# Kernel tuning notes

Hardware: AMD Instinct MI355X
Metric: run time of the kernel (lower is better)

The kernel has to match this reference:

```python
import jax, jax.numpy as jnp
import numpy as np

# DLMLayer (breadth=2) forward, soft/dense path.
# Group arities: 0 (nullary [B,C0]), 1 (unary [B,n,C1]), 2 (binary [B,n,n,C2]).
# Per group i: concat [Expand(inputs[i-1]), inputs[i], Reduce(inputs[i+1])],
# then Permutation(i) (concat over i! axis permutations), then logic MLP
# (Linear -> sigmoid) over the channel dim. exclude_self masks the diagonal
# in the binary->unary reduction (max filled with 0, min filled with 1,
# valid for probabilistic truth values in [0,1]).

def setup_inputs() -> dict:
    key = jax.random.key(0)
    ks = jax.random.split(key, 9)
    B, n, C = 16, 128, 64
    x0 = jax.random.uniform(ks[0], (B, 8), dtype=jnp.float32)
    x1 = jax.random.uniform(ks[1], (B, n, C), dtype=jnp.float32)
    x2 = jax.random.uniform(ks[2], (B, n, n, C), dtype=jnp.float32)
    # current_dim per group: i=0: 8 + 2*64 = 136 ; i=1: 8 + 64 + 2*64 = 200 (1!=1)
    # i=2: (64 + 64) * 2! = 256
    W0 = jax.random.normal(ks[3], (136, C), dtype=jnp.float32) * 0.1
    W1 = jax.random.normal(ks[4], (200, C), dtype=jnp.float32) * 0.1
    W2 = jax.random.normal(ks[5], (256, C), dtype=jnp.float32) * 0.1
    b0 = jnp.zeros((C,), jnp.float32)
    b1 = jnp.zeros((C,), jnp.float32)
    b2 = jnp.zeros((C,), jnp.float32)
    return {"x0": x0, "x1": x1, "x2": x2, "W0": W0, "b0": b0,
            "W1": W1, "b1": b1, "W2": W2, "b2": b2}


def reference(x0, x1, x2, W0, b0, W1, b1, W2, b2):
    B, n, C = x1.shape
    # ---- group 0 (nullary): input x0 + reduce(x1) over the object axis ----
    r1 = jnp.concatenate([x1.max(axis=1), x1.min(axis=1)], axis=-1)  # [B, 2C]
    f0 = jnp.concatenate([x0, r1], axis=-1)                          # [B, 136]
    out0 = jax.nn.sigmoid(f0 @ W0 + b0)                              # [B, C]
    # ---- group 1 (unary): expand x0, input x1, reduce x2 (exclude self) ----
    e0 = jnp.broadcast_to(x0[:, None, :], (B, n, x0.shape[-1]))      # [B, n, 8]
    diag = jnp.eye(n, dtype=bool)[None, :, :, None]                  # [1, n, n, 1]
    rmax = jnp.where(diag, 0.0, x2).max(axis=2)                      # [B, n, C]
    rmin = jnp.where(diag, 1.0, x2).min(axis=2)                      # [B, n, C]
    f1 = jnp.concatenate([e0, x1, rmax, rmin], axis=-1)              # [B, n, 200]
    out1 = jax.nn.sigmoid(f1 @ W1 + b1)                              # [B, n, C]
    # ---- group 2 (binary): expand x1, input x2, permute axes (1,2) ----
    e1 = jnp.broadcast_to(x1[:, :, None, :], (B, n, n, C))           # [B, n, n, C]
    g = jnp.concatenate([e1, x2], axis=-1)                           # [B, n, n, 2C]
    f2 = jnp.concatenate([g, jnp.swapaxes(g, 1, 2)], axis=-1)        # [B, n, n, 4C]
    out2 = jax.nn.sigmoid(f2 @ W2 + b2)                              # [B, n, n, C]
    return (out0, out1, out2)
```

## Files before the change

kernel.cpp:

```cpp
#include <hip/hip_runtime.h>
#include <hip/hip_bf16.h>
#include <cstdint>


#define NDIM 128
#define CDIM 64

typedef float f32x4 __attribute__((ext_vector_type(4)));
typedef short s16x8 __attribute__((ext_vector_type(8)));

__device__ __forceinline__ unsigned short f2bf(float f) {
    union { float f; unsigned int u; } v; v.f = f;
    unsigned int u = v.u;
    return (unsigned short)((u + 0x7FFFu + ((u >> 16) & 1u)) >> 16);
}
__device__ __forceinline__ float sigmoidf_(float x) {
    return 1.0f / (1.0f + __expf(-x));
}

__global__ void prep_pab(const float* __restrict__ x1, const float* __restrict__ W2,
                         const float* __restrict__ b2,
                         float* __restrict__ PA, float* __restrict__ PB) {
    int blk = blockIdx.x;
    int c = threadIdx.x;
    __shared__ float xv[64];
    xv[c] = x1[blk * 64 + c];
    __syncthreads();
    float accA = b2[c];
    float accB = 0.f;
#pragma unroll 8
    for (int k = 0; k < 64; ++k) {
        float xk = xv[k];
        accA += xk * W2[k * 64 + c];
        accB += xk * W2[(128 + k) * 64 + c];
    }
    PA[blk * 64 + c] = accA;
    PB[blk * 64 + c] = accB;
}

__global__ void prep_wt(const float* __restrict__ W2, unsigned short* __restrict__ WT) {
    int idx = blockIdx.x * 256 + threadIdx.x;
    int n = idx >> 7, k = idx & 127;
    int row = (k < 64) ? (64 + k) : (128 + k);
    WT[idx] = f2bf(W2[row * 64 + n]);
}

__global__ __launch_bounds__(256) void k_out0(const float* __restrict__ x0,
        const float* __restrict__ x1, const float* __restrict__ W0,
        const float* __restrict__ b0, float* __restrict__ out0) {
    int b = blockIdx.x;
    int t = threadIdx.x;
    int lane = t & 63, w = t >> 6;
    int q = lane & 15;
    int jq = lane >> 4;
    __shared__ float pw[4][64], pn[4][64], f0[136], spart[4][64];

    f32x4 mx = {-1e30f, -1e30f, -1e30f, -1e30f};
    f32x4 mn = {1e30f, 1e30f, 1e30f, 1e30f};
#pragma unroll
    for (int p = 0; p < 8; ++p) {
        int j = (w * 4 + jq) + 16 * p;
        float4 v = *reinterpret_cast<const float4*>(x1 + ((size_t)(b * 128 + j)) * 64 + q * 4);
        mx.x = fmaxf(mx.x, v.x); mx.y = fmaxf(mx.y, v.y);
        mx.z = fmaxf(mx.z, v.z); mx.w = fmaxf(mx.w, v.w);
        mn.x = fminf(mn.x, v.x); mn.y = fminf(mn.y, v.y);
        mn.z = fminf(mn.z, v.z); mn.w = fminf(mn.w, v.w);
    }
#pragma unroll
    for (int d = 16; d <= 32; d <<= 1) {
        mx.x = fmaxf(mx.x, __shfl_xor(mx.x, d)); mx.y = fmaxf(mx.y, __shfl_xor(mx.y, d));
        mx.z = fmaxf(mx.z, __shfl_xor(mx.z, d)); mx.w = fmaxf(mx.w, __shfl_xor(mx.w, d));
        mn.x = fminf(mn.x, __shfl_xor(mn.x, d)); mn.y = fminf(mn.y, __shfl_xor(mn.y, d));
        mn.z = fminf(mn.z, __shfl_xor(mn.z, d)); mn.w = fminf(mn.w, __shfl_xor(mn.w, d));
    }
    if (lane < 16) {
        *reinterpret_cast<f32x4*>(&pw[w][lane * 4]) = mx;
        *reinterpret_cast<f32x4*>(&pn[w][lane * 4]) = mn;
    }
    __syncthreads();
    if (t < 64) {
        int c = t;
        float M = fmaxf(fmaxf(pw[0][c], pw[1][c]), fmaxf(pw[2][c], pw[3][c]));
        float m = fminf(fminf(pn[0][c], pn[1][c]), fminf(pn[2][c], pn[3][c]));
        f0[8 + c] = M; f0[72 + c] = m;
        if (c < 8) f0[c] = x0[b * 8 + c];
    }
    __syncthreads();
    {
        int g = t >> 6, c = t & 63;
        float acc = 0.f;
#pragma unroll
        for (int k = g * 34; k < g * 34 + 34; ++k) acc += f0[k] * W0[k * 64 + c];
        spart[g][c] = acc;
    }
    __syncthreads();
    if (t < 64) {
        int c = t;
        out0[b * 64 + c] = sigmoidf_(spart[0][c] + spart[1][c] + spart[2][c] + spart[3][c] + b0[c]);
    }
}

__global__ __launch_bounds__(256) void k_fused(const float* __restrict__ x0,
        const float* __restrict__ x1, const float* __restrict__ x2,
        const unsigned short* __restrict__ WT,
        const float* __restrict__ W1, const float* __restrict__ b1,
        const float* __restrict__ PA, const float* __restrict__ PB,
        float* __restrict__ out1, float* __restrict__ out2) {
    int blk = blockIdx.x;
    int b = blk >> 7, i = blk & 127;
    int t = threadIdx.x;
    int lane = t & 63, w = t >> 6;
    int jq = lane >> 4;
    int cc = (lane & 15) * 4;

    __shared__ __align__(16) unsigned short Ald[128 * 128];
    __shared__ float pwmax[4][64], pwmin[4][64], spart[4][64], sf[200];

    const float* xaSrc = x2 + (size_t)blk * (NDIM * CDIM);

    float4 va[8];
#pragma unroll
    for (int p = 0; p < 8; ++p) {
        int j = 32 * w + p * 4 + jq;
        va[p] = *reinterpret_cast<const float4*>(xaSrc + j * 64 + cc);
    }
    f32x4 mx = {0.f, 0.f, 0.f, 0.f}, mn = {1.f, 1.f, 1.f, 1.f};
#pragma unroll
    for (int p = 0; p < 8; ++p) {
        int j = 32 * w + p * 4 + jq;
        bool ok = (j != i);
        float ax = ok ? va[p].x : 0.0f, ay = ok ? va[p].y : 0.0f;
        float az = ok ? va[p].z : 0.0f, aw = ok ? va[p].w : 0.0f;
        mx.x = fmaxf(mx.x, ax); mx.y = fmaxf(mx.y, ay);
        mx.z = fmaxf(mx.z, az); mx.w = fmaxf(mx.w, aw);
        float ix = ok ? va[p].x : 1.0f, iy = ok ? va[p].y : 1.0f;
        float iz = ok ? va[p].z : 1.0f, iw = ok ? va[p].w : 1.0f;
        mn.x = fminf(mn.x, ix); mn.y = fminf(mn.y, iy);
        mn.z = fminf(mn.z, iz); mn.w = fminf(mn.w, iw);
        ushort4 u;
        u.x = f2bf(va[p].x); u.y = f2bf(va[p].y); u.z = f2bf(va[p].z); u.w = f2bf(va[p].w);
        *reinterpret_cast<ushort4*>(&Ald[j * 128 + (cc ^ ((j & 7) << 3))]) = u;
    }
#pragma unroll
    for (int d = 16; d <= 32; d <<= 1) {
        mx.x = fmaxf(mx.x, __shfl_xor(mx.x, d)); mx.y = fmaxf(mx.y, __shfl_xor(mx.y, d));
        mx.z = fmaxf(mx.z, __shfl_xor(mx.z, d)); mx.w = fmaxf(mx.w, __shfl_xor(mx.w, d));
        mn.x = fminf(mn.x, __shfl_xor(mn.x, d)); mn.y = fminf(mn.y, __shfl_xor(mn.y, d));
        mn.z = fminf(mn.z, __shfl_xor(mn.z, d)); mn.w = fminf(mn.w, __shfl_xor(mn.w, d));
    }
    if (lane < 16) {
        *reinterpret_cast<f32x4*>(&pwmax[w][lane * 4]) = mx;
        *reinterpret_cast<f32x4*>(&pwmin[w][lane * 4]) = mn;
    }

#pragma unroll
    for (int p = 0; p < 8; ++p) {
        int j = 32 * w + p * 4 + jq;
        float4 v = *reinterpret_cast<const float4*>(
            x2 + ((size_t)((b * 128 + j) * 128 + i)) * 64 + cc);
        ushort4 u;
        u.x = f2bf(v.x); u.y = f2bf(v.y); u.z = f2bf(v.z); u.w = f2bf(v.w);
        *reinterpret_cast<ushort4*>(&Ald[j * 128 + ((64 + cc) ^ ((j & 7) << 3))]) = u;
    }

    s16x8 bfrag[4][4];
#pragma unroll
    for (int ks = 0; ks < 4; ++ks)
#pragma unroll
        for (int nt = 0; nt < 4; ++nt) {
            int n = nt * 16 + (lane & 15);
            int k0 = ks * 32 + (lane >> 4) * 8;
            bfrag[ks][nt] = *reinterpret_cast<const s16x8*>(WT + n * 128 + k0);
        }

    f32x4 acc[2][4];
#pragma unroll
    for (int m = 0; m < 2; ++m)
#pragma unroll
        for (int nt = 0; nt < 4; ++nt) acc[m][nt] = (f32x4){0.f, 0.f, 0.f, 0.f};

    asm volatile("s_waitcnt lgkmcnt(0)" ::: "memory");
    __builtin_amdgcn_sched_barrier(0);

#pragma unroll
    for (int ks = 0; ks < 4; ++ks) {
#pragma unroll
        for (int m = 0; m < 2; ++m) {
            int row = 32 * w + m * 16 + (lane & 15);
            int u8 = (ks * 4 + (lane >> 4)) * 8;
            s16x8 afrag = *reinterpret_cast<const s16x8*>(
                &Ald[row * 128 + (u8 ^ ((row & 7) << 3))]);
#pragma unroll
            for (int nt = 0; nt < 4; ++nt)
                acc[m][nt] = __builtin_amdgcn_mfma_f32_16x16x32_bf16(
                    afrag, bfrag[ks][nt], acc[m][nt], 0, 0, 0);
        }
    }

    const float* PBb = PB + b * 128 * 64;
    const float* PAi = PA + blk * 64;
    float* outBase = out2 + (size_t)blk * (NDIM * CDIM);
#pragma unroll
    for (int m = 0; m < 2; ++m) {
        int jt = 32 * w + m * 16 + (lane >> 4) * 4;
#pragma unroll
        for (int nt = 0; nt < 4; ++nt) {
            int cp = nt * 16 + (lane & 15);
            float pav = PAi[cp];
#pragma unroll
            for (int r = 0; r < 4; ++r) {
                int j = jt + r;
                outBase[j * 64 + cp] = sigmoidf_(acc[m][nt][r] + pav + PBb[j * 64 + cp]);
            }
        }
    }

    __syncthreads();
    int c = t & 63;
    if (t < 64) {
        float M = fmaxf(fmaxf(pwmax[0][c], pwmax[1][c]), fmaxf(pwmax[2][c], pwmax[3][c]));
        float m2 = fminf(fminf(pwmin[0][c], pwmin[1][c]), fminf(pwmin[2][c], pwmin[3][c]));
        sf[72 + c] = M; sf[136 + c] = m2;
        sf[8 + c] = x1[blk * 64 + c];
        if (c < 8) sf[c] = x0[b * 8 + c];
    }
    __syncthreads();
    {
        int g = t >> 6;
        float acc1 = 0.f;
#pragma unroll 10
        for (int k = g * 50; k < g * 50 + 50; ++k) acc1 += sf[k] * W1[k * 64 + c];
        spart[g][c] = acc1;
    }
    __syncthreads();
    if (t < 64) {
        out1[blk * 64 + c] = sigmoidf_(
            spart[0][c] + spart[1][c] + spart[2][c] + spart[3][c] + b1[c]);
    }
}

extern "C" void kernel_launch(void* const* d_in, const int* in_sizes, int n_in,
                              void* d_out, int out_size, void* d_ws, size_t ws_size,
                              hipStream_t stream) {
    const float* x0 = (const float*)d_in[0];
    const float* x1 = (const float*)d_in[1];
    const float* x2 = (const float*)d_in[2];
    const float* W0 = (const float*)d_in[3];
    const float* b0 = (const float*)d_in[4];
    const float* W1 = (const float*)d_in[5];
    const float* b1 = (const float*)d_in[6];
    const float* W2 = (const float*)d_in[7];
    const float* b2 = (const float*)d_in[8];

    float* out0 = (float*)d_out;
    float* out1 = out0 + 16 * 64;
    float* out2 = out1 + 16 * 128 * 64;

    float* PA = (float*)d_ws;
    float* PB = PA + 16 * 128 * 64;
    unsigned short* WT = (unsigned short*)(PB + 16 * 128 * 64);

    prep_pab<<<16 * 128, 64, 0, stream>>>(x1, W2, b2, PA, PB);
    prep_wt<<<32, 256, 0, stream>>>(W2, WT);
    k_out0<<<16, 256, 0, stream>>>(x0, x1, W0, b0, out0);
    k_fused<<<16 * 128, 256, 0, stream>>>(x0, x1, x2, WT, W1, b1, PA, PB, out1, out2);
}
```

Before: 60.62 us.

## Split fused kernel into half-row blocks and move out1 MLP to tail kernel

The main kernel now processes half of each (b,i) row per block, doubling the grid to 4096 blocks with half the LDS, and uses a remapped block index to interleave work across XCDs. Per-wave max/min partials go to a workspace, and a separate tail kernel reduces them and computes the unary-group MLP. B fragments are loaded per k-step instead of being held in registers, and launch bounds request higher occupancy. This aims at better occupancy and latency hiding, at the cost of an extra launch and a global round trip for the partial reductions.

Result: slower. 78.67 us (+29.8%).

```diff
diff --git a/kernel.cpp b/kernel.cpp
--- a/kernel.cpp
+++ b/kernel.cpp
@@ -100,46 +100,44 @@
     }
 }
 
-__global__ __launch_bounds__(256) void k_fused(const float* __restrict__ x0,
-        const float* __restrict__ x1, const float* __restrict__ x2,
+__global__ __launch_bounds__(256, 8) void k_fused(const float* __restrict__ x2,
         const unsigned short* __restrict__ WT,
-        const float* __restrict__ W1, const float* __restrict__ b1,
         const float* __restrict__ PA, const float* __restrict__ PB,
-        float* __restrict__ out1, float* __restrict__ out2) {
-    int blk = blockIdx.x;
+        float* __restrict__ pmax_ws, float* __restrict__ pmin_ws,
+        float* __restrict__ out2) {
+    int orig = blockIdx.x;
+    int blk2 = ((orig & 7) << 9) | (orig >> 3);
+    int blk = blk2 >> 1, half = blk2 & 1;
     int b = blk >> 7, i = blk & 127;
+    int j0 = half << 6;
     int t = threadIdx.x;
     int lane = t & 63, w = t >> 6;
     int jq = lane >> 4;
     int cc = (lane & 15) * 4;
 
-    __shared__ __align__(16) unsigned short Ald[128 * 128];
-    __shared__ float pwmax[4][64], pwmin[4][64], spart[4][64], sf[200];
+    __shared__ __align__(16) unsigned short Ald[64 * 128];
 
     const float* xaSrc = x2 + (size_t)blk * (NDIM * CDIM);
 
-    float4 va[8];
-#pragma unroll
-    for (int p = 0; p < 8; ++p) {
-        int j = 32 * w + p * 4 + jq;
+    float4 va[4];
+#pragma unroll
+    for (int p = 0; p < 4; ++p) {
+        int j = j0 + 16 * w + p * 4 + jq;
         va[p] = *reinterpret_cast<const float4*>(xaSrc + j * 64 + cc);
     }
     f32x4 mx = {0.f, 0.f, 0.f, 0.f}, mn = {1.f, 1.f, 1.f, 1.f};
 #pragma unroll
-    for (int p = 0; p < 8; ++p) {
-        int j = 32 * w + p * 4 + jq;
+    for (int p = 0; p < 4; ++p) {
+        int j = j0 + 16 * w + p * 4 + jq;
+        int jl = 16 * w + p * 4 + jq;
         bool ok = (j != i);
-        float ax = ok ? va[p].x : 0.0f, ay = ok ? va[p].y : 0.0f;
-        float az = ok ? va[p].z : 0.0f, aw = ok ? va[p].w : 0.0f;
-        mx.x = fmaxf(mx.x, ax); mx.y = fmaxf(mx.y, ay);
-        mx.z = fmaxf(mx.z, az); mx.w = fmaxf(mx.w, aw);
-        float ix = ok ? va[p].x : 1.0f, iy = ok ? va[p].y : 1.0f;
-        float iz = ok ? va[p].z : 1.0f, iw = ok ? va[p].w : 1.0f;
-        mn.x = fminf(mn.x, ix); mn.y = fminf(mn.y, iy);
-        mn.z = fminf(mn.z, iz); mn.w = fminf(mn.w, iw);
+        mx.x = fmaxf(mx.x, ok ? va[p].x : 0.0f); mx.y = fmaxf(mx.y, ok ? va[p].y : 0.0f);
+        mx.z = fmaxf(mx.z, ok ? va[p].z : 0.0f); mx.w = fmaxf(mx.w, ok ? va[p].w : 0.0f);
+        mn.x = fminf(mn.x, ok ? va[p].x : 1.0f); mn.y = fminf(mn.y, ok ? va[p].y : 1.0f);
+        mn.z = fminf(mn.z, ok ? va[p].z : 1.0f); mn.w = fminf(mn.w, ok ? va[p].w : 1.0f);
         ushort4 u;
         u.x = f2bf(va[p].x); u.y = f2bf(va[p].y); u.z = f2bf(va[p].z); u.w = f2bf(va[p].w);
-        *reinterpret_cast<ushort4*>(&Ald[j * 128 + (cc ^ ((j & 7) << 3))]) = u;
+        *reinterpret_cast<ushort4*>(&Ald[jl * 128 + (cc ^ ((jl & 7) << 3))]) = u;
     }
 #pragma unroll
     for (int d = 16; d <= 32; d <<= 1) {
@@ -149,88 +147,84 @@
         mn.z = fminf(mn.z, __shfl_xor(mn.z, d)); mn.w = fminf(mn.w, __shfl_xor(mn.w, d));
     }
     if (lane < 16) {
-        *reinterpret_cast<f32x4*>(&pwmax[w][lane * 4]) = mx;
-        *reinterpret_cast<f32x4*>(&pwmin[w][lane * 4]) = mn;
-    }
-
-#pragma unroll
-    for (int p = 0; p < 8; ++p) {
-        int j = 32 * w + p * 4 + jq;
+        int slot = blk2 * 4 + w;
+        *reinterpret_cast<f32x4*>(&pmax_ws[slot * 64 + lane * 4]) = mx;
+        *reinterpret_cast<f32x4*>(&pmin_ws[slot * 64 + lane * 4]) = mn;
+    }
+
+#pragma unroll
+    for (int p = 0; p < 4; ++p) {
+        int j = j0 + 16 * w + p * 4 + jq;
+        int jl = 16 * w + p * 4 + jq;
         float4 v = *reinterpret_cast<const float4*>(
             x2 + ((size_t)((b * 128 + j) * 128 + i)) * 64 + cc);
         ushort4 u;
         u.x = f2bf(v.x); u.y = f2bf(v.y); u.z = f2bf(v.z); u.w = f2bf(v.w);
-        *reinterpret_cast<ushort4*>(&Ald[j * 128 + ((64 + cc) ^ ((j & 7) << 3))]) = u;
-    }
-
-    s16x8 bfrag[4][4];
-#pragma unroll
-    for (int ks = 0; ks < 4; ++ks)
+        *reinterpret_cast<ushort4*>(&Ald[jl * 128 + ((64 + cc) ^ ((jl & 7) << 3))]) = u;
+    }
+
+    f32x4 acc[4];
+#pragma unroll
+    for (int nt = 0; nt < 4; ++nt) acc[nt] = (f32x4){0.f, 0.f, 0.f, 0.f};
+
+    asm volatile("s_waitcnt lgkmcnt(0)" ::: "memory");
+    __builtin_amdgcn_sched_barrier(0);
+
+    int rowl = 16 * w + (lane & 15);
+#pragma unroll
+    for (int ks = 0; ks < 4; ++ks) {
+        int u8 = (ks * 4 + jq) * 8;
+        s16x8 afrag = *reinterpret_cast<const s16x8*>(
+            &Ald[rowl * 128 + (u8 ^ ((rowl & 7) << 3))]);
 #pragma unroll
         for (int nt = 0; nt < 4; ++nt) {
             int n = nt * 16 + (lane & 15);
-            int k0 = ks * 32 + (lane >> 4) * 8;
-            bfrag[ks][nt] = *reinterpret_cast<const s16x8*>(WT + n * 128 + k0);
+            s16x8 bf = *reinterpret_cast<const s16x8*>(WT + n * 128 + ks * 32 + jq * 8);
+            acc[nt] = __builtin_amdgcn_mfma_f32_16x16x32_bf16(afrag, bf, acc[nt], 0, 0, 0);
         }
-
-    f32x4 acc[2][4];
-#pragma unroll
-    for (int m = 0; m < 2; ++m)
-#pragma unroll
-        for (int nt = 0; nt < 4; ++nt) acc[m][nt] = (f32x4){0.f, 0.f, 0.f, 0.f};
-
-    asm volatile("s_waitcnt lgkmcnt(0)" ::: "memory");
-    __builtin_amdgcn_sched_barrier(0);
-
-#pragma unroll
-    for (int ks = 0; ks < 4; ++ks) {
-#pragma unroll
-        for (int m = 0; m < 2; ++m) {
-            int row = 32 * w + m * 16 + (lane & 15);
-            int u8 = (ks * 4 + (lane >> 4)) * 8;
-            s16x8 afrag = *reinterpret_cast<const s16x8*>(
-                &Ald[row * 128 + (u8 ^ ((row & 7) << 3))]);
-#pragma unroll
-            for (int nt = 0; nt < 4; ++nt)
-                acc[m][nt] = __builtin_amdgcn_mfma_f32_16x16x32_bf16(
-                    afrag, bfrag[ks][nt], acc[m][nt], 0, 0, 0);
+    }
+
+    const float* PAi = PA + blk * 64;
+    const float* PBb = PB + b * 128 * 64;
+    float* outBase = out2 + (size_t)blk * (NDIM * CDIM);
+    int jt = j0 + 16 * w + jq * 4;
+#pragma unroll
+    for (int nt = 0; nt < 4; ++nt) {
+        int cp = nt * 16 + (lane & 15);
+        float pav = PAi[cp];
+#pragma unroll
+        for (int r = 0; r < 4; ++r) {
+            int j = jt + r;
+            outBase[j * 64 + cp] = sigmoidf_(acc[nt][r] + pav + PBb[j * 64 + cp]);
         }
     }
-
-    const float* PBb = PB + b * 128 * 64;
-    const float* PAi = PA + blk * 64;
-    float* outBase = out2 + (size_t)blk * (NDIM * CDIM);
-#pragma unroll
-    for (int m = 0; m < 2; ++m) {
-        int jt = 32 * w + m * 16 + (lane >> 4) * 4;
-#pragma unroll
-        for (int nt = 0; nt < 4; ++nt) {
-            int cp = nt * 16 + (lane & 15);
-            float pav = PAi[cp];
-#pragma unroll
-            for (int r = 0; r < 4; ++r) {
-                int j = jt + r;
-                outBase[j * 64 + cp] = sigmoidf_(acc[m][nt][r] + pav + PBb[j * 64 + cp]);
-            }
+}
+
+__global__ __launch_bounds__(256) void k_out1_tail(const float* __restrict__ x0,
+        const float* __restrict__ x1, const float* __restrict__ W1,
+        const float* __restrict__ b1, const float* __restrict__ pmax_ws,
+        const float* __restrict__ pmin_ws, float* __restrict__ out1) {
+    int blk = blockIdx.x;
+    int t = threadIdx.x;
+    int c = t & 63, g = t >> 6;
+    __shared__ float sf[200], spart[4][64];
+    if (t < 64) {
+        float M = 0.f, m = 1.f;
+#pragma unroll
+        for (int s = 0; s < 8; ++s) {
+            M = fmaxf(M, pmax_ws[(blk * 8 + s) * 64 + c]);
+            m = fminf(m, pmin_ws[(blk * 8 + s) * 64 + c]);
         }
-    }
-
-    __syncthreads();
-    int c = t & 63;
-    if (t < 64) {
-        float M = fmaxf(fmaxf(pwmax[0][c], pwmax[1][c]), fmaxf(pwmax[2][c], pwmax[3][c]));
-        float m2 = fminf(fminf(pwmin[0][c], pwmin[1][c]), fminf(pwmin[2][c], pwmin[3][c]));
-        sf[72 + c] = M; sf[136 + c] = m2;
+        sf[72 + c] = M; sf[136 + c] = m;
         sf[8 + c] = x1[blk * 64 + c];
-        if (c < 8) sf[c] = x0[b * 8 + c];
+        if (c < 8) sf[c] = x0[(blk >> 7) * 8 + c];
     }
     __syncthreads();
     {
-        int g = t >> 6;
-        float acc1 = 0.f;
+        float a = 0.f;
 #pragma unroll 10
-        for (int k = g * 50; k < g * 50 + 50; ++k) acc1 += sf[k] * W1[k * 64 + c];
-        spart[g][c] = acc1;
+        for (int k = g * 50; k < g * 50 + 50; ++k) a += sf[k] * W1[k * 64 + c];
+        spart[g][c] = a;
     }
     __syncthreads();
     if (t < 64) {
@@ -259,9 +253,12 @@
     float* PA = (float*)d_ws;
     float* PB = PA + 16 * 128 * 64;
     unsigned short* WT = (unsigned short*)(PB + 16 * 128 * 64);
+    float* pmax_ws = (float*)(WT + 64 * 128);
+    float* pmin_ws = pmax_ws + 16384 * 64;
 
     prep_pab<<<16 * 128, 64, 0, stream>>>(x1, W2, b2, PA, PB);
     prep_wt<<<32, 256, 0, stream>>>(W2, WT);
     k_out0<<<16, 256, 0, stream>>>(x0, x1, W0, b0, out0);
-    k_fused<<<16 * 128, 256, 0, stream>>>(x0, x1, x2, WT, W1, b1, PA, PB, out1, out2);
-}
+    k_fused<<<4096, 256, 0, stream>>>(x2, WT, PA, PB, pmax_ws, pmin_ws, out2);
+    k_out1_tail<<<16 * 128, 256, 0, stream>>>(x0, x1, W1, b1, pmax_ws, pmin_ws, out1);
+}
```

## Merge prep kernels, alias LDS buffers, add XCD-aware block swizzle

Applied to the files above, without the earlier changes.

The three small setup kernels (PA/PB projection, bf16 weight transpose, out0) become one launch, with block ranges picking the role. This removes two kernel launches and their serialization. In the main kernel, the reduction and partial-sum scratch now aliases the bf16 A tile in one 32 KB LDS buffer, and launch bounds request 5 blocks per CU, to raise occupancy. Block indices are remapped so each group of eight consecutive launch IDs spreads across XCDs, giving each XCD a contiguous slice of the (b,i) range for better L2 reuse of the transposed x2 reads. The trade-off is that the max/min partials stay live in registers across the MFMA phase, adding register pressure under the tighter bound, plus an extra barrier.

Measured after the change: 68.39 us. 12.8% more time.

```diff
diff --git a/kernel.cpp b/kernel.cpp
--- a/kernel.cpp
+++ b/kernel.cpp
@@ -18,53 +18,128 @@
     return 1.0f / (1.0f + __expf(-x));
 }
 
-__global__ void prep_pab(const float* __restrict__ x1, const float* __restrict__ W2,
-                         const float* __restrict__ b2,
-                         float* __restrict__ PA, float* __restrict__ PB) {
-    int blk = blockIdx.x;
-    int c = threadIdx.x;
-    __shared__ float xv[64];
-    xv[c] = x1[blk * 64 + c];
-    __syncthreads();
-    float accA = b2[c];
-    float accB = 0.f;
+__global__ __launch_bounds__(256) void k_prep(const float* __restrict__ x0,
+        const float* __restrict__ x1, const float* __restrict__ W0,
+        const float* __restrict__ b0, const float* __restrict__ W2,
+        const float* __restrict__ b2, float* __restrict__ PA,
+        float* __restrict__ PB, unsigned short* __restrict__ WT,
+        float* __restrict__ out0) {
+    int bb = blockIdx.x;
+    int t = threadIdx.x;
+    if (bb < 512) {
+        int u = t >> 6, c = t & 63;
+        int blk = bb * 4 + u;
+        __shared__ float xv[4][64];
+        xv[u][c] = x1[blk * 64 + c];
+        float accA = b2[c];
+        float accB = 0.f;
 #pragma unroll 8
-    for (int k = 0; k < 64; ++k) {
-        float xk = xv[k];
-        accA += xk * W2[k * 64 + c];
-        accB += xk * W2[(128 + k) * 64 + c];
-    }
-    PA[blk * 64 + c] = accA;
-    PB[blk * 64 + c] = accB;
-}
-
-__global__ void prep_wt(const float* __restrict__ W2, unsigned short* __restrict__ WT) {
-    int idx = blockIdx.x * 256 + threadIdx.x;
-    int n = idx >> 7, k = idx & 127;
-    int row = (k < 64) ? (64 + k) : (128 + k);
-    WT[idx] = f2bf(W2[row * 64 + n]);
-}
-
-__global__ __launch_bounds__(256) void k_out0(const float* __restrict__ x0,
-        const float* __restrict__ x1, const float* __restrict__ W0,
-        const float* __restrict__ b0, float* __restrict__ out0) {
-    int b = blockIdx.x;
+        for (int k = 0; k < 64; ++k) {
+            float xk = xv[u][k];
+            accA += xk * W2[k * 64 + c];
+            accB += xk * W2[(128 + k) * 64 + c];
+        }
+        PA[blk * 64 + c] = accA;
+        PB[blk * 64 + c] = accB;
+    } else if (bb < 544) {
+        int idx = (bb - 512) * 256 + t;
+        int n = idx >> 7, k = idx & 127;
+        int row = (k < 64) ? (64 + k) : (128 + k);
+        WT[idx] = f2bf(W2[row * 64 + n]);
+    } else {
+        int b = bb - 544;
+        int lane = t & 63, w = t >> 6;
+        int q = lane & 15;
+        int jq = lane >> 4;
+        __shared__ float pw[4][64], pn[4][64], f0[136], spart[4][64];
+        f32x4 mx = {-1e30f, -1e30f, -1e30f, -1e30f};
+        f32x4 mn = {1e30f, 1e30f, 1e30f, 1e30f};
+#pragma unroll
+        for (int p = 0; p < 8; ++p) {
+            int j = (w * 4 + jq) + 16 * p;
+            float4 v = *reinterpret_cast<const float4*>(
+                x1 + ((size_t)(b * 128 + j)) * 64 + q * 4);
+            mx.x = fmaxf(mx.x, v.x); mx.y = fmaxf(mx.y, v.y);
+            mx.z = fmaxf(mx.z, v.z); mx.w = fmaxf(mx.w, v.w);
+            mn.x = fminf(mn.x, v.x); mn.y = fminf(mn.y, v.y);
+            mn.z = fminf(mn.z, v.z); mn.w = fminf(mn.w, v.w);
+        }
+#pragma unroll
+        for (int d = 16; d <= 32; d <<= 1) {
+            mx.x = fmaxf(mx.x, __shfl_xor(mx.x, d)); mx.y = fmaxf(mx.y, __shfl_xor(mx.y, d));
+            mx.z = fmaxf(mx.z, __shfl_xor(mx.z, d)); mx.w = fmaxf(mx.w, __shfl_xor(mx.w, d));
+            mn.x = fminf(mn.x, __shfl_xor(mn.x, d)); mn.y = fminf(mn.y, __shfl_xor(mn.y, d));
+            mn.z = fminf(mn.z, __shfl_xor(mn.z, d)); mn.w = fminf(mn.w, __shfl_xor(mn.w, d));
+        }
+        if (lane < 16) {
+            *reinterpret_cast<f32x4*>(&pw[w][lane * 4]) = mx;
+            *reinterpret_cast<f32x4*>(&pn[w][lane * 4]) = mn;
+        }
+        __syncthreads();
+        if (t < 64) {
+            int c = t;
+            float M = fmaxf(fmaxf(pw[0][c], pw[1][c]), fmaxf(pw[2][c], pw[3][c]));
+            float m = fminf(fminf(pn[0][c], pn[1][c]), fminf(pn[2][c], pn[3][c]));
+            f0[8 + c] = M; f0[72 + c] = m;
+            if (c < 8) f0[c] = x0[b * 8 + c];
+        }
+        __syncthreads();
+        {
+            int g = t >> 6, c = t & 63;
+            float acc = 0.f;
+#pragma unroll
+            for (int k = g * 34; k < g * 34 + 34; ++k) acc += f0[k] * W0[k * 64 + c];
+            spart[g][c] = acc;
+        }
+        __syncthreads();
+        if (t < 64) {
+            int c = t;
+            out0[b * 64 + c] = sigmoidf_(
+                spart[0][c] + spart[1][c] + spart[2][c] + spart[3][c] + b0[c]);
+        }
+    }
+}
+
+__global__ __launch_bounds__(256, 5) void k_fused(const float* __restrict__ x0,
+        const float* __restrict__ x1, const float* __restrict__ x2,
+        const unsigned short* __restrict__ WT,
+        const float* __restrict__ W1, const float* __restrict__ b1,
+        const float* __restrict__ PA, const float* __restrict__ PB,
+        float* __restrict__ out1, float* __restrict__ out2) {
+    int blk = ((blockIdx.x & 7) << 8) | (blockIdx.x >> 3);
+    int b = blk >> 7, i = blk & 127;
     int t = threadIdx.x;
     int lane = t & 63, w = t >> 6;
-    int q = lane & 15;
     int jq = lane >> 4;
-    __shared__ float pw[4][64], pn[4][64], f0[136], spart[4][64];
-
-    f32x4 mx = {-1e30f, -1e30f, -1e30f, -1e30f};
-    f32x4 mn = {1e30f, 1e30f, 1e30f, 1e30f};
+    int cc = (lane & 15) * 4;
+
+    __shared__ __align__(16) unsigned char shraw[32768];
+    unsigned short* Ald = reinterpret_cast<unsigned short*>(shraw);
+    float* sfT = reinterpret_cast<float*>(shraw);
+    float* spartT = sfT + 256;
+    float* pwT = spartT + 256;
+    float* pnT = pwT + 256;
+
+    const float* xaSrc = x2 + (size_t)blk * (NDIM * CDIM);
+
+    float4 va[8];
 #pragma unroll
     for (int p = 0; p < 8; ++p) {
-        int j = (w * 4 + jq) + 16 * p;
-        float4 v = *reinterpret_cast<const float4*>(x1 + ((size_t)(b * 128 + j)) * 64 + q * 4);
-        mx.x = fmaxf(mx.x, v.x); mx.y = fmaxf(mx.y, v.y);
-        mx.z = fmaxf(mx.z, v.z); mx.w = fmaxf(mx.w, v.w);
-        mn.x = fminf(mn.x, v.x); mn.y = fminf(mn.y, v.y);
-        mn.z = fminf(mn.z, v.z); mn.w = fminf(mn.w, v.w);
+        int j = 32 * w + p * 4 + jq;
+        va[p] = *reinterpret_cast<const float4*>(xaSrc + j * 64 + cc);
+    }
+    f32x4 mx = {0.f, 0.f, 0.f, 0.f}, mn = {1.f, 1.f, 1.f, 1.f};
+#pragma unroll
+    for (int p = 0; p < 8; ++p) {
+        int j = 32 * w + p * 4 + jq;
+        bool ok = (j != i);
+        mx.x = fmaxf(mx.x, ok ? va[p].x : 0.0f); mx.y = fmaxf(mx.y, ok ? va[p].y : 0.0f);
+        mx.z = fmaxf(mx.z, ok ? va[p].z : 0.0f); mx.w = fmaxf(mx.w, ok ? va[p].w : 0.0f);
+        mn.x = fminf(mn.x, ok ? va[p].x : 1.0f); mn.y = fminf(mn.y, ok ? va[p].y : 1.0f);
+        mn.z = fminf(mn.z, ok ? va[p].z : 1.0f); mn.w = fminf(mn.w, ok ? va[p].w : 1.0f);
+        ushort4 u;
+        u.x = f2bf(va[p].x); u.y = f2bf(va[p].y); u.z = f2bf(va[p].z); u.w = f2bf(va[p].w);
+        *reinterpret_cast<ushort4*>(&Ald[j * 128 + (cc ^ ((j & 7) << 3))]) = u;
     }
 #pragma unroll
     for (int d = 16; d <= 32; d <<= 1) {
@@ -72,85 +147,6 @@
         mx.z = fmaxf(mx.z, __shfl_xor(mx.z, d)); mx.w = fmaxf(mx.w, __shfl_xor(mx.w, d));
         mn.x = fminf(mn.x, __shfl_xor(mn.x, d)); mn.y = fminf(mn.y, __shfl_xor(mn.y, d));
         mn.z = fminf(mn.z, __shfl_xor(mn.z, d)); mn.w = fminf(mn.w, __shfl_xor(mn.w, d));
-    }
-    if (lane < 16) {
-        *reinterpret_cast<f32x4*>(&pw[w][lane * 4]) = mx;
-        *reinterpret_cast<f32x4*>(&pn[w][lane * 4]) = mn;
-    }
-    __syncthreads();
-    if (t < 64) {
-        int c = t;
-        float M = fmaxf(fmaxf(pw[0][c], pw[1][c]), fmaxf(pw[2][c], pw[3][c]));
-        float m = fminf(fminf(pn[0][c], pn[1][c]), fminf(pn[2][c], pn[3][c]));
-        f0[8 + c] = M; f0[72 + c] = m;
-        if (c < 8) f0[c] = x0[b * 8 + c];
-    }
-    __syncthreads();
-    {
-        int g = t >> 6, c = t & 63;
-        float acc = 0.f;
-#pragma unroll
-        for (int k = g * 34; k < g * 34 + 34; ++k) acc += f0[k] * W0[k * 64 + c];
-        spart[g][c] = acc;
-    }
-    __syncthreads();
-    if (t < 64) {
-        int c = t;
-        out0[b * 64 + c] = sigmoidf_(spart[0][c] + spart[1][c] + spart[2][c] + spart[3][c] + b0[c]);
-    }
-}
-
-__global__ __launch_bounds__(256) void k_fused(const float* __restrict__ x0,
-        const float* __restrict__ x1, const float* __restrict__ x2,
-        const unsigned short* __restrict__ WT,
-        const float* __restrict__ W1, const float* __restrict__ b1,
-        const float* __restrict__ PA, const float* __restrict__ PB,
-        float* __restrict__ out1, float* __restrict__ out2) {
-    int blk = blockIdx.x;
-    int b = blk >> 7, i = blk & 127;
-    int t = threadIdx.x;
-    int lane = t & 63, w = t >> 6;
-    int jq = lane >> 4;
-    int cc = (lane & 15) * 4;
-
-    __shared__ __align__(16) unsigned short Ald[128 * 128];
-    __shared__ float pwmax[4][64], pwmin[4][64], spart[4][64], sf[200];
-
-    const float* xaSrc = x2 + (size_t)blk * (NDIM * CDIM);
-
-    float4 va[8];
-#pragma unroll
-    for (int p = 0; p < 8; ++p) {
-        int j = 32 * w + p * 4 + jq;
-        va[p] = *reinterpret_cast<const float4*>(xaSrc + j * 64 + cc);
-    }
-    f32x4 mx = {0.f, 0.f, 0.f, 0.f}, mn = {1.f, 1.f, 1.f, 1.f};
-#pragma unroll
-    for (int p = 0; p < 8; ++p) {
-        int j = 32 * w + p * 4 + jq;
-        bool ok = (j != i);
-        float ax = ok ? va[p].x : 0.0f, ay = ok ? va[p].y : 0.0f;
-        float az = ok ? va[p].z : 0.0f, aw = ok ? va[p].w : 0.0f;
-        mx.x = fmaxf(mx.x, ax); mx.y = fmaxf(mx.y, ay);
-        mx.z = fmaxf(mx.z, az); mx.w = fmaxf(mx.w, aw);
-        float ix = ok ? va[p].x : 1.0f, iy = ok ? va[p].y : 1.0f;
-        float iz = ok ? va[p].z : 1.0f, iw = ok ? va[p].w : 1.0f;
-        mn.x = fminf(mn.x, ix); mn.y = fminf(mn.y, iy);
-        mn.z = fminf(mn.z, iz); mn.w = fminf(mn.w, iw);
-        ushort4 u;
-        u.x = f2bf(va[p].x); u.y = f2bf(va[p].y); u.z = f2bf(va[p].z); u.w = f2bf(va[p].w);
-        *reinterpret_cast<ushort4*>(&Ald[j * 128 + (cc ^ ((j & 7) << 3))]) = u;
-    }
-#pragma unroll
-    for (int d = 16; d <= 32; d <<= 1) {
-        mx.x = fmaxf(mx.x, __shfl_xor(mx.x, d)); mx.y = fmaxf(mx.y, __shfl_xor(mx.y, d));
-        mx.z = fmaxf(mx.z, __shfl_xor(mx.z, d)); mx.w = fmaxf(mx.w, __shfl_xor(mx.w, d));
-        mn.x = fminf(mn.x, __shfl_xor(mn.x, d)); mn.y = fminf(mn.y, __shfl_xor(mn.y, d));
-        mn.z = fminf(mn.z, __shfl_xor(mn.z, d)); mn.w = fminf(mn.w, __shfl_xor(mn.w, d));
-    }
-    if (lane < 16) {
-        *reinterpret_cast<f32x4*>(&pwmax[w][lane * 4]) = mx;
-        *reinterpret_cast<f32x4*>(&pwmin[w][lane * 4]) = mn;
     }
 
 #pragma unroll
@@ -169,7 +165,7 @@
 #pragma unroll
         for (int nt = 0; nt < 4; ++nt) {
             int n = nt * 16 + (lane & 15);
-            int k0 = ks * 32 + (lane >> 4) * 8;
+            int k0 = ks * 32 + jq * 8;
             bfrag[ks][nt] = *reinterpret_cast<const s16x8*>(WT + n * 128 + k0);
         }
 
@@ -187,7 +183,7 @@
 #pragma unroll
         for (int m = 0; m < 2; ++m) {
             int row = 32 * w + m * 16 + (lane & 15);
-            int u8 = (ks * 4 + (lane >> 4)) * 8;
+            int u8 = (ks * 4 + jq) * 8;
             s16x8 afrag = *reinterpret_cast<const s16x8*>(
                 &Ald[row * 128 + (u8 ^ ((row & 7) << 3))]);
 #pragma unroll
@@ -197,12 +193,12 @@
         }
     }
 
+    const float* PAi = PA + blk * 64;
     const float* PBb = PB + b * 128 * 64;
-    const float* PAi = PA + blk * 64;
     float* outBase = out2 + (size_t)blk * (NDIM * CDIM);
 #pragma unroll
     for (int m = 0; m < 2; ++m) {
-        int jt = 32 * w + m * 16 + (lane >> 4) * 4;
+        int jt = 32 * w + m * 16 + jq * 4;
 #pragma unroll
         for (int nt = 0; nt < 4; ++nt) {
             int cp = nt * 16 + (lane & 15);
@@ -216,26 +212,31 @@
     }
 
     __syncthreads();
+    if (lane < 16) {
+        *reinterpret_cast<f32x4*>(&pwT[w * 64 + lane * 4]) = mx;
+        *reinterpret_cast<f32x4*>(&pnT[w * 64 + lane * 4]) = mn;
+    }
+    __syncthreads();
     int c = t & 63;
     if (t < 64) {
-        float M = fmaxf(fmaxf(pwmax[0][c], pwmax[1][c]), fmaxf(pwmax[2][c], pwmax[3][c]));
-        float m2 = fminf(fminf(pwmin[0][c], pwmin[1][c]), fminf(pwmin[2][c], pwmin[3][c]));
-        sf[72 + c] = M; sf[136 + c] = m2;
-        sf[8 + c] = x1[blk * 64 + c];
-        if (c < 8) sf[c] = x0[b * 8 + c];
+        float M = fmaxf(fmaxf(pwT[c], pwT[64 + c]), fmaxf(pwT[128 + c], pwT[192 + c]));
+        float m2 = fminf(fminf(pnT[c], pnT[64 + c]), fminf(pnT[128 + c], pnT[192 + c]));
+        sfT[72 + c] = M; sfT[136 + c] = m2;
+        sfT[8 + c] = x1[blk * 64 + c];
+        if (c < 8) sfT[c] = x0[b * 8 + c];
     }
     __syncthreads();
     {
         int g = t >> 6;
         float acc1 = 0.f;
 #pragma unroll 10
-        for (int k = g * 50; k < g * 50 + 50; ++k) acc1 += sf[k] * W1[k * 64 + c];
-        spart[g][c] = acc1;
+        for (int k = g * 50; k < g * 50 + 50; ++k) acc1 += sfT[k] * W1[k * 64 + c];
+        spartT[g * 64 + c] = acc1;
     }
     __syncthreads();
     if (t < 64) {
         out1[blk * 64 + c] = sigmoidf_(
-            spart[0][c] + spart[1][c] + spart[2][c] + spart[3][c] + b1[c]);
+            spartT[c] + spartT[64 + c] + spartT[128 + c] + spartT[192 + c] + b1[c]);
     }
 }
 
@@ -260,8 +261,6 @@
     float* PB = PA + 16 * 128 * 64;
     unsigned short* WT = (unsigned short*)(PB + 16 * 128 * 64);
 
-    prep_pab<<<16 * 128, 64, 0, stream>>>(x1, W2, b2, PA, PB);
-    prep_wt<<<32, 256, 0, stream>>>(W2, WT);
-    k_out0<<<16, 256, 0, stream>>>(x0, x1, W0, b0, out0);
-    k_fused<<<16 * 128, 256, 0, stream>>>(x0, x1, x2, WT, W1, b1, PA, PB, out1, out2);
-}
+    k_prep<<<560, 256, 0, stream>>>(x0, x1, W0, b0, W2, b2, PA, PB, WT, out0);
+    k_fused<<<2048, 256, 0, stream>>>(x0, x1, x2, WT, W1, b1, PA, PB, out1, out2);
+}
```
